# Performance work log

Measured on AMD Instinct MI355X. Metric: run time of the kernel, lower is better.

Reference implementation:

```python
import jax, jax.numpy as jnp
import numpy as np

B, S, H, NH = 4, 1024, 1024, 16
DH = H // NH
EPS = 1e-12  # BERT layer_norm_eps


def layer_norm(x, scale, bias, eps=EPS):
    mu = jnp.mean(x, axis=-1, keepdims=True)
    var = jnp.var(x, axis=-1, keepdims=True)
    return (x - mu) / jnp.sqrt(var + eps) * scale + bias


def setup_inputs() -> dict:
    key = jax.random.key(0)
    ks = jax.random.split(key, 8)
    lin = lambda k: jax.random.normal(k, (H, H), jnp.float32) * 0.02
    zeros_h = jnp.zeros((H,), jnp.float32)
    return {
        "hidden_states": jax.random.normal(ks[0], (B, S, H), jnp.float32),
        "group_prob": jnp.zeros((B, S, S), jnp.float32),
        "attention_mask": jnp.ones((B, 1, S, S), jnp.int32),
        "Wq": lin(ks[1]), "bq": zeros_h,
        "Wk": lin(ks[2]), "bk": zeros_h,
        "Wv": lin(ks[3]), "bv": zeros_h,
        "gWq": lin(ks[4]), "gbq": zeros_h,
        "gWk": lin(ks[5]), "gbk": zeros_h,
        "g_ln_scale": jnp.ones((H,), jnp.float32), "g_ln_bias": zeros_h,
        "Wo": lin(ks[6]), "bo": zeros_h,
        "out_ln_scale": jnp.ones((H,), jnp.float32), "out_ln_bias": zeros_h,
    }


def _forward(hidden_states, group_prob, attention_mask, Wq, bq, Wk, bk, Wv, bv,
             gWq, gbq, gWk, gbk, g_ln_scale, g_ln_bias, Wo, bo,
             out_ln_scale, out_ln_bias):
    am = attention_mask.astype(jnp.int32)              # [B,1,S,S]
    a = jnp.eye(S, k=1, dtype=jnp.int32)               # superdiagonal
    b = jnp.eye(S, dtype=jnp.int32)                    # identity
    c = jnp.eye(S, k=-1, dtype=jnp.int32)              # subdiagonal
    tri = jnp.triu(jnp.ones((S, S), jnp.float32))      # upper tri incl diag

    # ---- GroupAttention (tree-transformer constituent priors) ----
    hs = layer_norm(hidden_states, g_ln_scale, g_ln_bias)
    gq = hs @ gWq.T + gbq
    gk = hs @ gWk.T + gbk
    g_scores = jnp.einsum('bqd,bkd->bqk', gq, gk) / jnp.float32(H)
    g_mask = (am & (a + c))[:, 0]                      # [B,S,S] tridiag band, no diag
    g_scores = jnp.where(g_mask == 0, -jnp.inf, g_scores)
    n_attn = jnp.nan_to_num(jax.nn.softmax(g_scores, axis=-1))
    n_attn = jnp.sqrt(n_attn * jnp.swapaxes(n_attn, -1, -2) + 1e-9)
    n_attn = group_prob + (1.0 - group_prob) * n_attn  # prior mixing
    t = jnp.where(a == 0, 0.0, jnp.log(n_attn + 1e-9)) @ tri
    g_attn = jnp.exp(tri @ t)
    strict_upper = tri.astype(jnp.int32) - b           # nonzero on strict upper tri
    g_attn = jnp.where(strict_upper == 0, 0.0, g_attn)
    g_attn = g_attn + jnp.swapaxes(g_attn, -1, -2) + jnp.where(b == 0, 1e-9, n_attn)
    break_prob = n_attn

    # ---- BertSelfAttention, mode 'L' ----
    def split_heads(x):
        return x.reshape(B, S, NH, DH).transpose(0, 2, 1, 3)  # [B,NH,S,DH]
    q = split_heads(hidden_states @ Wq.T + bq)
    k = split_heads(hidden_states @ Wk.T + bk)
    v = split_heads(hidden_states @ Wv.T + bv)
    scores = jnp.einsum('bhqd,bhkd->bhqk', q, k) / jnp.sqrt(jnp.float32(DH))
    keep = (am | b) != 0                               # diag always attended
    scores = jnp.where(keep, scores, -jnp.inf)
    probs = jax.nn.softmax(scores, axis=-1)
    probs = probs * g_attn[:, None]                    # group-prob reweighting
    ctx = jnp.einsum('bhqk,bhkd->bhqd', probs, v)
    ctx = ctx.transpose(0, 2, 1, 3).reshape(B, S, H)

    # ---- BertSelfOutput: dense + residual + LayerNorm ----
    out = layer_norm(ctx @ Wo.T + bo + hidden_states, out_ln_scale, out_ln_bias)
    return out, scores, g_attn, break_prob


def reference(hidden_states, group_prob, attention_mask, Wq, bq, Wk, bk, Wv, bv,
              gWq, gbq, gWk, gbk, g_ln_scale, g_ln_bias, Wo, bo,
              out_ln_scale, out_ln_bias):
    return _forward(hidden_states, group_prob, attention_mask, Wq, bq, Wk, bk,
                    Wv, bv, gWq, gbq, gWk, gbk, g_ln_scale, g_ln_bias, Wo, bo,
                    out_ln_scale, out_ln_bias)
```

## Files before the change

kernel.cpp:

```cpp
#include <hip/hip_runtime.h>
#include <math.h>

#define BB 4
#define S 1024
#define H 1024
#define NHD 16
#define DH 64
#define LN_EPS 1e-12f
#define SQ9 3.1622776601683795e-5f
#define NEG_INF (-__builtin_inff())

typedef unsigned short u16;
typedef unsigned int u32;
using bfrag = __attribute__((ext_vector_type(8))) short;
using f32x4 = __attribute__((ext_vector_type(4))) float;

typedef __attribute__((address_space(1))) void void_g;
typedef __attribute__((address_space(3))) void void_l;

__device__ __forceinline__ void gload16(const void* g, void* l) {
  __builtin_amdgcn_global_load_lds((void_g*)g, (void_l*)l, 16, 0, 0);
}

__device__ __forceinline__ u16 f2bf(float f) {
  u32 u = __builtin_bit_cast(u32, f);
  u32 r = (u + 0x7fffu + ((u >> 16) & 1u)) >> 16;
  return (u16)r;
}
__device__ __forceinline__ float bf2f(u32 b) {
  u32 u = b << 16;
  return __builtin_bit_cast(float, u);
}

__device__ __forceinline__ float block_sum256(float v, float* buf) {
#pragma unroll
  for (int o = 32; o > 0; o >>= 1) v += __shfl_down(v, o);
  if ((threadIdx.x & 63) == 0) buf[threadIdx.x >> 6] = v;
  __syncthreads();
  float r = buf[0] + buf[1] + buf[2] + buf[3];
  __syncthreads();
  return r;
}

__global__ __launch_bounds__(256) void prep_kernel(
    const float* __restrict__ Wq, const float* __restrict__ Wk, const float* __restrict__ Wv,
    const float* __restrict__ gWq, const float* __restrict__ gWk,
    const float* __restrict__ hidden, const int* __restrict__ am,
    const float* __restrict__ glns, const float* __restrict__ glnb,
    u16* __restrict__ dstW, u32* __restrict__ amb, u16* __restrict__ hsbf) {
  __shared__ float buf[4];
  int bid = blockIdx.x;
  if (bid < 9216) {
    const int WQ = 262144;
    int i = bid * 256 + threadIdx.x;
    const float* src; int off;
    if      (i < 1 * WQ) { src = Wq;  off = 0; }
    else if (i < 2 * WQ) { src = Wk;  off = 1 * WQ; }
    else if (i < 3 * WQ) { src = Wv;  off = 2 * WQ; }
    else if (i < 4 * WQ) { src = gWq; off = 3 * WQ; }
    else if (i < 5 * WQ) { src = gWk; off = 4 * WQ; }
    else                 { src = hidden; off = 5 * WQ; }
    float4 v = reinterpret_cast<const float4*>(src)[i - off];
    u32 lo = (u32)f2bf(v.x) | ((u32)f2bf(v.y) << 16);
    u32 hi = (u32)f2bf(v.z) | ((u32)f2bf(v.w) << 16);
    reinterpret_cast<uint2*>(dstW)[i] = make_uint2(lo, hi);
  } else if (bid < 25600) {
    size_t t = (size_t)(bid - 9216) * 256 + threadIdx.x;
    int v = am[t] != 0;
    unsigned long long m = __ballot(v);
    int lane = threadIdx.x & 63;
    if (lane == 0)       amb[t >> 5] = (u32)m;
    else if (lane == 32) amb[t >> 5] = (u32)(m >> 32);
  } else {
    size_t row = bid - 25600;
    const float4 xv = reinterpret_cast<const float4*>(hidden + row * H)[threadIdx.x];
    float s  = xv.x + xv.y + xv.z + xv.w;
    float s2 = xv.x * xv.x + xv.y * xv.y + xv.z * xv.z + xv.w * xv.w;
    s  = block_sum256(s, buf);
    s2 = block_sum256(s2, buf);
    float mu  = s * (1.0f / H);
    float var = s2 * (1.0f / H) - mu * mu;
    float inv = rsqrtf(var + LN_EPS);
    const float4 sv = reinterpret_cast<const float4*>(glns)[threadIdx.x];
    const float4 bv = reinterpret_cast<const float4*>(glnb)[threadIdx.x];
    float o0 = (xv.x - mu) * inv * sv.x + bv.x;
    float o1 = (xv.y - mu) * inv * sv.y + bv.y;
    float o2 = (xv.z - mu) * inv * sv.z + bv.z;
    float o3 = (xv.w - mu) * inv * sv.w + bv.w;
    u32 lo = (u32)f2bf(o0) | ((u32)f2bf(o1) << 16);
    u32 hi = (u32)f2bf(o2) | ((u32)f2bf(o3) << 16);
    reinterpret_cast<uint2*>(hsbf + row * H)[threadIdx.x] = make_uint2(lo, hi);
  }
}

__global__ __launch_bounds__(256) void cast_wo_kernel(const float* __restrict__ Wo,
                                                      u16* __restrict__ dst) {
  int i = blockIdx.x * 256 + threadIdx.x;
  float4 v = reinterpret_cast<const float4*>(Wo)[i];
  u32 lo = (u32)f2bf(v.x) | ((u32)f2bf(v.y) << 16);
  u32 hi = (u32)f2bf(v.z) | ((u32)f2bf(v.w) << 16);
  reinterpret_cast<uint2*>(dst)[i] = make_uint2(lo, hi);
}

__global__ __launch_bounds__(256) void mega_gemm(
    const u16* __restrict__ hbf, const u16* __restrict__ hsbf,
    const u16* __restrict__ Wcat,
    const float* __restrict__ bq, const float* __restrict__ bk, const float* __restrict__ bv,
    const float* __restrict__ gbq, const float* __restrict__ gbk,
    u16* __restrict__ q, u16* __restrict__ k, u16* __restrict__ vt,
    u16* __restrict__ gq, u16* __restrict__ gk) {
  __shared__ __align__(16) u16 SM[32768];
  const int Kdim = H;
  int fid = blockIdx.x + blockIdx.y * 40;
  int swz = (fid & 7) * 160 + (fid >> 3);
  int lx = swz % 40, ly = swz / 40;
  int which = lx >> 3;
  const u16* A = (which < 3) ? hbf : hsbf;
  int rowBlk = ly * 128, colBlk = lx * 128;
  int tid = threadIdx.x, wid = tid >> 6, l = tid & 63;
  int dr = l >> 3, sl = l & 7;
  int co = (sl ^ dr) << 3;
  const u16* Ag = A + (size_t)rowBlk * Kdim;
  const u16* Bg = Wcat + (size_t)colBlk * Kdim;
  f32x4 acc[4][4];
#pragma unroll
  for (int i = 0; i < 4; ++i)
#pragma unroll
    for (int j = 0; j < 4; ++j) acc[i][j] = (f32x4){0.f, 0.f, 0.f, 0.f};
#pragma unroll
  for (int i = 0; i < 4; ++i) {
    int L = wid * 4 + i;
    gload16(Ag + (size_t)(L * 8 + dr) * Kdim + co, &SM[L * 512]);
    gload16(Bg + (size_t)(L * 8 + dr) * Kdim + co, &SM[16384 + L * 512]);
  }
  __syncthreads();
  int wm = wid >> 1, wn = wid & 1;
  const int nt = Kdim >> 6;
  int buf = 0;
  int sw = (l & 7) << 4;
  for (int t = 0; t < nt; ++t) {
    if (t + 1 < nt) {
      int k0 = (t + 1) << 6;
      int dstoff = (buf ^ 1) * 8192;
#pragma unroll
      for (int i = 0; i < 4; ++i) {
        int L = wid * 4 + i;
        gload16(Ag + (size_t)(L * 8 + dr) * Kdim + k0 + co, &SM[dstoff + L * 512]);
        gload16(Bg + (size_t)(L * 8 + dr) * Kdim + k0 + co, &SM[16384 + dstoff + L * 512]);
      }
    }
    const char* Ab = (const char*)&SM[buf * 8192];
    const char* Bb = (const char*)&SM[16384 + buf * 8192];
#pragma unroll
    for (int ks = 0; ks < 2; ++ks) {
      int kb = (ks * 64 + ((l >> 4) << 4)) ^ sw;
      bfrag af[4], bfv[4];
#pragma unroll
      for (int mi = 0; mi < 4; ++mi)
        af[mi] = *(const bfrag*)(Ab + (wm * 64 + mi * 16 + (l & 15)) * 128 + kb);
#pragma unroll
      for (int ni = 0; ni < 4; ++ni)
        bfv[ni] = *(const bfrag*)(Bb + (wn * 64 + ni * 16 + (l & 15)) * 128 + kb);
#pragma unroll
      for (int mi = 0; mi < 4; ++mi)
#pragma unroll
        for (int ni = 0; ni < 4; ++ni)
          acc[mi][ni] = __builtin_amdgcn_mfma_f32_16x16x32_bf16(af[mi], bfv[ni], acc[mi][ni], 0, 0, 0);
    }
    __syncthreads();
    buf ^= 1;
  }
  const float* bias = (which == 0) ? bq : (which == 1) ? bk : (which == 2) ? bv
                      : (which == 3) ? gbq : gbk;
  if (which == 2) {
    u16* T = SM;
#pragma unroll
    for (int mi = 0; mi < 4; ++mi) {
#pragma unroll
      for (int ni = 0; ni < 4; ++ni) {
        int c = wn * 64 + ni * 16 + (l & 15);
        float bvv = bias[(colBlk & 1023) + c];
        int tokb = wm * 64 + mi * 16 + ((l >> 4) << 2);
        u32 w0 = (u32)f2bf(acc[mi][ni][0] + bvv) | ((u32)f2bf(acc[mi][ni][1] + bvv) << 16);
        u32 w1 = (u32)f2bf(acc[mi][ni][2] + bvv) | ((u32)f2bf(acc[mi][ni][3] + bvv) << 16);
        *(u32*)&T[c * 144 + tokb]     = w0;
        *(u32*)&T[c * 144 + tokb + 2] = w1;
      }
    }
    __syncthreads();
    int col = tid >> 1, th = tid & 1;
    int g = (colBlk & 1023) + col;
    int bb = rowBlk >> 10;
    int s0 = (rowBlk & 1023) + th * 64;
    const uint4* src = (const uint4*)&T[col * 144 + th * 64];
    u16* dst = vt + ((size_t)(bb * 1024 + g)) * S + s0;
#pragma unroll
    for (int i = 0; i < 8; ++i) reinterpret_cast<uint4*>(dst)[i] = src[i];
  } else {
    u16* O = (which == 0) ? q : (which == 1) ? k : (which == 3) ? gq : gk;
#pragma unroll
    for (int mi = 0; mi < 4; ++mi) {
#pragma unroll
      for (int ni = 0; ni < 4; ++ni) {
        int col = (colBlk + wn * 64 + ni * 16 + (l & 15)) & 1023;
        float bvv = bias[col];
#pragma unroll
        for (int j = 0; j < 4; ++j) {
          int row = rowBlk + wm * 64 + mi * 16 + ((l >> 4) << 2) + j;
          O[(size_t)row * H + col] = f2bf(acc[mi][ni][j] + bvv);
        }
      }
    }
  }
}

__global__ __launch_bounds__(256) void gemm_dense(
    const u16* __restrict__ A, const u16* __restrict__ Bw,
    const float* __restrict__ bias, const float* __restrict__ resid,
    u16* __restrict__ C) {
  __shared__ __align__(16) u16 SM[32768];
  const int Kdim = H;
  int fid = blockIdx.x + blockIdx.y * 8;
  int swz = (fid & 7) * 32 + (fid >> 3);
  int lx = swz & 7, ly = swz >> 3;
  int rowBlk = ly * 128, colBlk = lx * 128;
  int tid = threadIdx.x, wid = tid >> 6, l = tid & 63;
  int dr = l >> 3, sl = l & 7;
  int co = (sl ^ dr) << 3;
  const u16* Ag = A + (size_t)rowBlk * Kdim;
  const u16* Bg = Bw + (size_t)colBlk * Kdim;
  f32x4 acc[4][4];
#pragma unroll
  for (int i = 0; i < 4; ++i)
#pragma unroll
    for (int j = 0; j < 4; ++j) acc[i][j] = (f32x4){0.f, 0.f, 0.f, 0.f};
#pragma unroll
  for (int i = 0; i < 4; ++i) {
    int L = wid * 4 + i;
    gload16(Ag + (size_t)(L * 8 + dr) * Kdim + co, &SM[L * 512]);
    gload16(Bg + (size_t)(L * 8 + dr) * Kdim + co, &SM[16384 + L * 512]);
  }
  __syncthreads();
  int wm = wid >> 1, wn = wid & 1;
  const int nt = Kdim >> 6;
  int buf = 0;
  int sw = (l & 7) << 4;
  for (int t = 0; t < nt; ++t) {
    if (t + 1 < nt) {
      int k0 = (t + 1) << 6;
      int dstoff = (buf ^ 1) * 8192;
#pragma unroll
      for (int i = 0; i < 4; ++i) {
        int L = wid * 4 + i;
        gload16(Ag + (size_t)(L * 8 + dr) * Kdim + k0 + co, &SM[dstoff + L * 512]);
        gload16(Bg + (size_t)(L * 8 + dr) * Kdim + k0 + co, &SM[16384 + dstoff + L * 512]);
      }
    }
    const char* Ab = (const char*)&SM[buf * 8192];
    const char* Bb = (const char*)&SM[16384 + buf * 8192];
#pragma unroll
    for (int ks = 0; ks < 2; ++ks) {
      int kb = (ks * 64 + ((l >> 4) << 4)) ^ sw;
      bfrag af[4], bfv[4];
#pragma unroll
      for (int mi = 0; mi < 4; ++mi)
        af[mi] = *(const bfrag*)(Ab + (wm * 64 + mi * 16 + (l & 15)) * 128 + kb);
#pragma unroll
      for (int ni = 0; ni < 4; ++ni)
        bfv[ni] = *(const bfrag*)(Bb + (wn * 64 + ni * 16 + (l & 15)) * 128 + kb);
#pragma unroll
      for (int mi = 0; mi < 4; ++mi)
#pragma unroll
        for (int ni = 0; ni < 4; ++ni)
          acc[mi][ni] = __builtin_amdgcn_mfma_f32_16x16x32_bf16(af[mi], bfv[ni], acc[mi][ni], 0, 0, 0);
    }
    __syncthreads();
    buf ^= 1;
  }
#pragma unroll
  for (int mi = 0; mi < 4; ++mi) {
#pragma unroll
    for (int ni = 0; ni < 4; ++ni) {
      int col = colBlk + wn * 64 + ni * 16 + (l & 15);
      float bvv = bias[col];
#pragma unroll
      for (int j = 0; j < 4; ++j) {
        int row = rowBlk + wm * 64 + mi * 16 + ((l >> 4) << 2) + j;
        C[(size_t)row * H + col] = f2bf(acc[mi][ni][j] + bvv + resid[(size_t)row * H + col]);
      }
    }
  }
}

__global__ __launch_bounds__(256) void band_dots_kernel(
    const u16* __restrict__ gq, const u16* __restrict__ gk,
    float* __restrict__ znext, float* __restrict__ zprev) {
  __shared__ float buf[4];
  size_t idx = blockIdx.x;
  int i = (int)(idx & (S - 1));
  uint2 q2 = reinterpret_cast<const uint2*>(gq + idx * H)[threadIdx.x];
  float q0 = bf2f(q2.x & 0xffff), q1 = bf2f(q2.x >> 16);
  float q2f = bf2f(q2.y & 0xffff), q3 = bf2f(q2.y >> 16);
  float dn = 0.f, dp = 0.f;
  if (i < S - 1) {
    uint2 k2 = reinterpret_cast<const uint2*>(gk + (idx + 1) * H)[threadIdx.x];
    dn = q0 * bf2f(k2.x & 0xffff) + q1 * bf2f(k2.x >> 16) +
         q2f * bf2f(k2.y & 0xffff) + q3 * bf2f(k2.y >> 16);
  }
  if (i > 0) {
    uint2 k2 = reinterpret_cast<const uint2*>(gk + (idx - 1) * H)[threadIdx.x];
    dp = q0 * bf2f(k2.x & 0xffff) + q1 * bf2f(k2.x >> 16) +
         q2f * bf2f(k2.y & 0xffff) + q3 * bf2f(k2.y >> 16);
  }
  dn = block_sum256(dn, buf);
  dp = block_sum256(dp, buf);
  if (threadIdx.x == 0) { znext[idx] = dn; zprev[idx] = dp; }
}

__global__ __launch_bounds__(1024) void band_prefix_kernel(
    const float* __restrict__ znext, const float* __restrict__ zprev,
    const int* __restrict__ am, const float* __restrict__ gp,
    float* __restrict__ sband, float* __restrict__ Cpre) {
  __shared__ float pd[S];
  __shared__ float scn[S];
  int b = blockIdx.x, i = threadIdx.x;
  size_t idx = (size_t)b * S + i;
  bool luv = (i < S - 1) && (am[((size_t)b * S + i) * S + i + 1] != 0);
  bool ldv = (i > 0) && (am[((size_t)b * S + i) * S + i - 1] != 0);
  float pf, pdn;
  if (!luv && !ldv) { pf = 0.f; pdn = 0.f; }
  else if (!ldv)    { pf = 1.f; pdn = 0.f; }
  else if (!luv)    { pf = 0.f; pdn = 1.f; }
  else {
    float lu = znext[idx] * (1.0f / (float)H);
    float ld = zprev[idx] * (1.0f / (float)H);
    float m = fmaxf(lu, ld);
    float eu = expf(lu - m), ed = expf(ld - m);
    float inv = 1.f / (eu + ed);
    pf = eu * inv; pdn = ed * inv;
  }
  pd[i] = pdn;
  __syncthreads();
  float sb = 0.f, L = 0.f;
  if (i < S - 1) {
    sb = sqrtf(pf * pd[i + 1] + 1e-9f);
    float gpv = gp[((size_t)b * S + i) * S + (i + 1)];
    float nm = gpv + (1.f - gpv) * sb;
    L = logf(nm + 1e-9f);
  }
  sband[idx] = sb;
  scn[i] = L;
  __syncthreads();
  for (int off = 1; off < S; off <<= 1) {
    float t = (i >= off) ? scn[i - off] : 0.f;
    __syncthreads();
    scn[i] += t;
    __syncthreads();
  }
  Cpre[idx] = (i > 0) ? scn[i - 1] : 0.f;
}

__global__ __launch_bounds__(256) void gattn_write_kernel(
    const float* __restrict__ gp, const float* __restrict__ sband,
    const float* __restrict__ Cpre, float* __restrict__ ga, float* __restrict__ brk) {
  __shared__ float Crow[S];
  __shared__ float Srow[S];
  size_t bi = blockIdx.x;
  int b = (int)(bi >> 10), i = (int)(bi & (S - 1));
  reinterpret_cast<float4*>(Crow)[threadIdx.x] =
      reinterpret_cast<const float4*>(Cpre + (size_t)b * S)[threadIdx.x];
  reinterpret_cast<float4*>(Srow)[threadIdx.x] =
      reinterpret_cast<const float4*>(sband + (size_t)b * S)[threadIdx.x];
  __syncthreads();
  float Ci = Crow[i];
  size_t rowoff = bi * S;
  const float4 g4 = reinterpret_cast<const float4*>(gp + rowoff)[threadIdx.x];
  const float gparr[4] = {g4.x, g4.y, g4.z, g4.w};
  float go[4], bo_[4];
#pragma unroll
  for (int j = 0; j < 4; ++j) {
    int k = threadIdx.x * 4 + j;
    float gpv = gparr[j];
    float gav;
    if (k == i) {
      gav = gpv + (1.f - gpv) * SQ9;
    } else {
      float d = (k > i) ? (Crow[k] - Ci) : (Ci - Crow[k]);
      gav = expf(d) + 1e-9f;
    }
    float sval = (k == i + 1) ? Srow[i] : ((k == i - 1) ? Srow[k] : SQ9);
    go[j]  = gav;
    bo_[j] = gpv + (1.f - gpv) * sval;
  }
  f32x4 go4 = (f32x4){go[0], go[1], go[2], go[3]};
  __builtin_nontemporal_store(go4, reinterpret_cast<f32x4*>(ga + rowoff) + threadIdx.x);
  f32x4 bo4 = (f32x4){bo_[0], bo_[1], bo_[2], bo_[3]};
  __builtin_nontemporal_store(bo4, reinterpret_cast<f32x4*>(brk + rowoff) + threadIdx.x);
}

__global__ __launch_bounds__(256) void flash_kernel(
    const u16* __restrict__ q, const u16* __restrict__ k, const u16* __restrict__ vt,
    const u32* __restrict__ amb, const float* __restrict__ Cpre,
    const float* __restrict__ gp,
    float* __restrict__ scores, u16* __restrict__ ctx) {
  __shared__ __align__(16) u16 Qt[4096];
  __shared__ __align__(16) u16 Kt[2][4096];
  __shared__ __align__(16) u16 Vt[2][4096];
  __shared__ __align__(16) u16 Pt[4096];
  __shared__ float CLds[1024];
  int fid = blockIdx.x + blockIdx.y * 16;
  int swz = (fid & 7) * 128 + (fid >> 3);
  int qb = swz & 15, bh = swz >> 4;
  int b = bh >> 4, h = bh & 15;
  int tid = threadIdx.x, wid = tid >> 6, l = tid & 63;
  int dr = l >> 3, sl = l & 7;
  int co = (sl ^ dr) << 3;
  const u16* qbase = q + ((size_t)b * S + qb * 64) * H + h * 64;
  const u16* kbase = k + (size_t)b * S * H + h * 64;
  const u16* vtb   = vt + (size_t)bh * 64 * S;
  reinterpret_cast<float4*>(CLds)[tid] =
      reinterpret_cast<const float4*>(Cpre + (size_t)b * S)[tid];
#pragma unroll
  for (int i = 0; i < 2; ++i) {
    int L = wid * 2 + i;
    gload16(qbase + (size_t)(L * 8 + dr) * H + co, &Qt[L * 512]);
    gload16(kbase + (size_t)(L * 8 + dr) * H + co, &Kt[0][L * 512]);
    gload16(vtb + (size_t)(L * 8 + dr) * S + co, &Vt[0][L * 512]);
  }
  __syncthreads();
  int sw = (l & 7) << 4;
  int qr = l & 15;
  bfrag qa[2];
#pragma unroll
  for (int ks = 0; ks < 2; ++ks) {
    int kb = (ks * 64 + ((l >> 4) << 4)) ^ sw;
    qa[ks] = *(const bfrag*)((const char*)Qt + (wid * 16 + qr) * 128 + kb);
  }
  int rowg0 = qb * 64 + wid * 16 + ((l >> 4) << 2);
  float Ci[4], gdiag[4];
#pragma unroll
  for (int j = 0; j < 4; ++j) {
    int row = rowg0 + j;
    Ci[j] = CLds[row];
    float gpd = gp[((size_t)b * S + row) * S + row];
    gdiag[j] = gpd + (1.f - gpd) * SQ9;
  }
  float m_run[4], l_run[4];
  f32x4 oacc[4];
#pragma unroll
  for (int j = 0; j < 4; ++j) { m_run[j] = NEG_INF; l_run[j] = 0.f; }
#pragma unroll
  for (int nb = 0; nb < 4; ++nb) oacc[nb] = (f32x4){0.f, 0.f, 0.f, 0.f};
  int buf = 0;
  for (int kt = 0; kt < 16; ++kt) {
    if (kt < 15) {
      const u16* kb2 = kbase + (size_t)((kt + 1) * 64) * H;
#pragma unroll
      for (int i = 0; i < 2; ++i) {
        int L = wid * 2 + i;
        gload16(kb2 + (size_t)(L * 8 + dr) * H + co, &Kt[buf ^ 1][L * 512]);
        gload16(vtb + (size_t)(L * 8 + dr) * S + (kt + 1) * 64 + co, &Vt[buf ^ 1][L * 512]);
      }
    }
    f32x4 acc[4];
#pragma unroll
    for (int nb = 0; nb < 4; ++nb) acc[nb] = (f32x4){0.f, 0.f, 0.f, 0.f};
#pragma unroll
    for (int ks = 0; ks < 2; ++ks) {
      int kb = (ks * 64 + ((l >> 4) << 4)) ^ sw;
#pragma unroll
      for (int nb = 0; nb < 4; ++nb) {
        bfrag bv = *(const bfrag*)((const char*)Kt[buf] + (nb * 16 + qr) * 128 + kb);
        acc[nb] = __builtin_amdgcn_mfma_f32_16x16x32_bf16(qa[ks], bv, acc[nb], 0, 0, 0);
      }
    }
    float vals[4][4];
    float tm[4] = {NEG_INF, NEG_INF, NEG_INF, NEG_INF};
#pragma unroll
    for (int j = 0; j < 4; ++j) {
      int row = rowg0 + j;
      const u32* amw = amb + ((size_t)b * S + row) * 32 + kt * 2;
      u32 w0 = amw[0], w1 = amw[1];
      float* srow = scores + ((size_t)bh * S + row) * S + kt * 64;
#pragma unroll
      for (int nb = 0; nb < 4; ++nb) {
        int col = nb * 16 + qr;
        int colg = kt * 64 + col;
        u32 word = (nb < 2) ? w0 : w1;
        int keep = (int)((word >> (col & 31)) & 1u) | (row == colg);
        float v = keep ? acc[nb][j] * 0.125f : NEG_INF;
        vals[nb][j] = v;
        __builtin_nontemporal_store(v, srow + col);
        tm[j] = fmaxf(tm[j], v);
      }
    }
#pragma unroll
    for (int j = 0; j < 4; ++j) {
#pragma unroll
      for (int o = 1; o < 16; o <<= 1) tm[j] = fmaxf(tm[j], __shfl_xor(tm[j], o));
    }
    float Ck[4];
#pragma unroll
    for (int nb = 0; nb < 4; ++nb) Ck[nb] = CLds[kt * 64 + nb * 16 + qr];
#pragma unroll
    for (int j = 0; j < 4; ++j) {
      int row = rowg0 + j;
      int prow = wid * 16 + ((l >> 4) << 2) + j;
      char* ptrow = (char*)Pt + prow * 128;
      int psw = (prow & 7) << 4;
      float mn = fmaxf(m_run[j], tm[j]);
      float p[4];
      float sc = 1.f, lsum = 0.f;
      if (mn > NEG_INF) {
        sc = expf(m_run[j] - mn);
#pragma unroll
        for (int nb = 0; nb < 4; ++nb) p[nb] = expf(vals[nb][j] - mn);
        lsum = p[0] + p[1] + p[2] + p[3];
      } else {
#pragma unroll
        for (int nb = 0; nb < 4; ++nb) p[nb] = 0.f;
      }
#pragma unroll
      for (int o = 1; o < 16; o <<= 1) lsum += __shfl_xor(lsum, o);
      m_run[j] = mn;
      l_run[j] = l_run[j] * sc + lsum;
#pragma unroll
      for (int nb = 0; nb < 4; ++nb) {
        int colg = kt * 64 + nb * 16 + qr;
        bool isdiag = (colg == row);
        float d = (colg > row) ? (Ck[nb] - Ci[j]) : (Ci[j] - Ck[nb]);
        float gaval = isdiag ? gdiag[j] : expf(d);
        float pg = p[nb] * gaval;
        *(u16*)(ptrow + (((nb * 16 + qr) * 2) ^ psw)) = f2bf(pg);
        oacc[nb][j] *= sc;
      }
    }
#pragma unroll
    for (int ks = 0; ks < 2; ++ks) {
      int kb = (ks * 64 + ((l >> 4) << 4)) ^ sw;
      bfrag pa = *(const bfrag*)((const char*)Pt + (wid * 16 + qr) * 128 + kb);
#pragma unroll
      for (int nb = 0; nb < 4; ++nb) {
        bfrag vv = *(const bfrag*)((const char*)Vt[buf] + (nb * 16 + qr) * 128 + kb);
        oacc[nb] = __builtin_amdgcn_mfma_f32_16x16x32_bf16(pa, vv, oacc[nb], 0, 0, 0);
      }
    }
    __syncthreads();
    buf ^= 1;
  }
#pragma unroll
  for (int j = 0; j < 4; ++j) {
    int row = rowg0 + j;
    float ir = 1.f / l_run[j];
#pragma unroll
    for (int nb = 0; nb < 4; ++nb) {
      int d = nb * 16 + qr;
      ctx[((size_t)b * S + row) * H + h * 64 + d] = f2bf(oacc[nb][j] * ir);
    }
  }
}

__global__ __launch_bounds__(256) void ln_bf_kernel(
    const u16* __restrict__ x, const float* __restrict__ sc,
    const float* __restrict__ bi, float* __restrict__ y) {
  __shared__ float buf[4];
  size_t row = blockIdx.x;
  uint2 xv = reinterpret_cast<const uint2*>(x + row * H)[threadIdx.x];
  float x0 = bf2f(xv.x & 0xffff), x1 = bf2f(xv.x >> 16);
  float x2 = bf2f(xv.y & 0xffff), x3 = bf2f(xv.y >> 16);
  float s  = x0 + x1 + x2 + x3;
  float s2 = x0 * x0 + x1 * x1 + x2 * x2 + x3 * x3;
  s  = block_sum256(s, buf);
  s2 = block_sum256(s2, buf);
  float mu  = s * (1.0f / H);
  float var = s2 * (1.0f / H) - mu * mu;
  float inv = rsqrtf(var + LN_EPS);
  const float4 sv = reinterpret_cast<const float4*>(sc)[threadIdx.x];
  const float4 bv = reinterpret_cast<const float4*>(bi)[threadIdx.x];
  float4 o;
  o.x = (x0 - mu) * inv * sv.x + bv.x;
  o.y = (x1 - mu) * inv * sv.y + bv.y;
  o.z = (x2 - mu) * inv * sv.z + bv.z;
  o.w = (x3 - mu) * inv * sv.w + bv.w;
  reinterpret_cast<float4*>(y + row * H)[threadIdx.x] = o;
}

extern "C" void kernel_launch(void* const* d_in, const int* in_sizes, int n_in,
                              void* d_out, int out_size, void* d_ws, size_t ws_size,
                              hipStream_t stream) {
  const float* hidden = (const float*)d_in[0];
  const float* gp     = (const float*)d_in[1];
  const int*   am     = (const int*)d_in[2];
  const float* Wq = (const float*)d_in[3];  const float* bq = (const float*)d_in[4];
  const float* Wk = (const float*)d_in[5];  const float* bk = (const float*)d_in[6];
  const float* Wv = (const float*)d_in[7];  const float* bv = (const float*)d_in[8];
  const float* gWq = (const float*)d_in[9]; const float* gbq = (const float*)d_in[10];
  const float* gWk = (const float*)d_in[11];const float* gbk = (const float*)d_in[12];
  const float* glns = (const float*)d_in[13]; const float* glnb = (const float*)d_in[14];
  const float* Wo = (const float*)d_in[15]; const float* bo = (const float*)d_in[16];
  const float* olns = (const float*)d_in[17]; const float* olnb = (const float*)d_in[18];

  float* out    = (float*)d_out;
  float* scores = out + (size_t)BB * S * H;
  float* gattn  = scores + (size_t)BB * NHD * S * S;
  float* brk    = gattn + (size_t)BB * S * S;

  const size_t MB = 1u << 20;
  char* w = (char*)d_ws;
  u16* Wcat  = (u16*)(w);
  u16* hbf   = (u16*)(w + 10 * MB);
  u16* ctxbf = hbf;
  u16* hsbf  = (u16*)(w + 18 * MB);
  u16* Wobf  = hsbf;
  u16* qbf   = (u16*)(w + 26 * MB);
  u16* kbf   = (u16*)(w + 34 * MB);
  u16* vtb   = (u16*)(w + 42 * MB);
  u16* gqbf  = (u16*)(w + 50 * MB);
  u16* densebf = gqbf;
  u16* gkbf  = (u16*)(w + 58 * MB);
  u32* amb   = (u32*)(w + 66 * MB);
  float* znext  = (float*)(w + 66 * MB + 512 * 1024);
  float* zprev  = znext + BB * S;
  float* sbandA = zprev + BB * S;
  float* CpreA  = sbandA + BB * S;

  dim3 blk(256);

  prep_kernel<<<29696, blk, 0, stream>>>(Wq, Wk, Wv, gWq, gWk, hidden, am,
                                         glns, glnb, Wcat, amb, hsbf);

  mega_gemm<<<dim3(40, 32), blk, 0, stream>>>(hbf, hsbf, Wcat,
                                              bq, bk, bv, gbq, gbk,
                                              qbf, kbf, vtb, gqbf, gkbf);
  cast_wo_kernel<<<1024, blk, 0, stream>>>(Wo, Wobf);

  band_dots_kernel<<<BB * S, blk, 0, stream>>>(gqbf, gkbf, znext, zprev);
  band_prefix_kernel<<<BB, 1024, 0, stream>>>(znext, zprev, am, gp, sbandA, CpreA);
  gattn_write_kernel<<<BB * S, blk, 0, stream>>>(gp, sbandA, CpreA, gattn, brk);

  flash_kernel<<<dim3(16, 64), blk, 0, stream>>>(qbf, kbf, vtb, amb, CpreA, gp,
                                                 scores, ctxbf);

  gemm_dense<<<dim3(8, 32), blk, 0, stream>>>(ctxbf, Wobf, bo, hidden, densebf);
  ln_bf_kernel<<<BB * S, blk, 0, stream>>>(densebf, olns, olnb, out);
}
```

Before: 273.5 us.

## Fuse group-attention and break-prob writes into flash kernel head-0 blocks

Removes the separate gattn_write kernel. The flash-attention blocks for head 0 of each batch now compute and write g_attn and break_prob rows tile by tile alongside their attention work. The block-to-tile mapping changes so that the head-0 blocks, which carry the extra work, are scheduled first. This saves one kernel launch and overlaps the memory-bound output writes with compute-bound attention. The cost is load imbalance: 64 blocks do extra global traffic and exp work, and shared memory per block grows.

```diff
diff --git a/kernel.cpp b/kernel.cpp
--- a/kernel.cpp
+++ b/kernel.cpp
@@ -360,57 +360,28 @@
   Cpre[idx] = (i > 0) ? scn[i - 1] : 0.f;
 }
 
-__global__ __launch_bounds__(256) void gattn_write_kernel(
-    const float* __restrict__ gp, const float* __restrict__ sband,
-    const float* __restrict__ Cpre, float* __restrict__ ga, float* __restrict__ brk) {
-  __shared__ float Crow[S];
-  __shared__ float Srow[S];
-  size_t bi = blockIdx.x;
-  int b = (int)(bi >> 10), i = (int)(bi & (S - 1));
-  reinterpret_cast<float4*>(Crow)[threadIdx.x] =
-      reinterpret_cast<const float4*>(Cpre + (size_t)b * S)[threadIdx.x];
-  reinterpret_cast<float4*>(Srow)[threadIdx.x] =
-      reinterpret_cast<const float4*>(sband + (size_t)b * S)[threadIdx.x];
-  __syncthreads();
-  float Ci = Crow[i];
-  size_t rowoff = bi * S;
-  const float4 g4 = reinterpret_cast<const float4*>(gp + rowoff)[threadIdx.x];
-  const float gparr[4] = {g4.x, g4.y, g4.z, g4.w};
-  float go[4], bo_[4];
-#pragma unroll
-  for (int j = 0; j < 4; ++j) {
-    int k = threadIdx.x * 4 + j;
-    float gpv = gparr[j];
-    float gav;
-    if (k == i) {
-      gav = gpv + (1.f - gpv) * SQ9;
-    } else {
-      float d = (k > i) ? (Crow[k] - Ci) : (Ci - Crow[k]);
-      gav = expf(d) + 1e-9f;
-    }
-    float sval = (k == i + 1) ? Srow[i] : ((k == i - 1) ? Srow[k] : SQ9);
-    go[j]  = gav;
-    bo_[j] = gpv + (1.f - gpv) * sval;
-  }
-  f32x4 go4 = (f32x4){go[0], go[1], go[2], go[3]};
-  __builtin_nontemporal_store(go4, reinterpret_cast<f32x4*>(ga + rowoff) + threadIdx.x);
-  f32x4 bo4 = (f32x4){bo_[0], bo_[1], bo_[2], bo_[3]};
-  __builtin_nontemporal_store(bo4, reinterpret_cast<f32x4*>(brk + rowoff) + threadIdx.x);
-}
-
 __global__ __launch_bounds__(256) void flash_kernel(
     const u16* __restrict__ q, const u16* __restrict__ k, const u16* __restrict__ vt,
     const u32* __restrict__ amb, const float* __restrict__ Cpre,
-    const float* __restrict__ gp,
-    float* __restrict__ scores, u16* __restrict__ ctx) {
+    const float* __restrict__ sband, const float* __restrict__ gp,
+    float* __restrict__ scores, u16* __restrict__ ctx,
+    float* __restrict__ ga, float* __restrict__ brk) {
   __shared__ __align__(16) u16 Qt[4096];
   __shared__ __align__(16) u16 Kt[2][4096];
   __shared__ __align__(16) u16 Vt[2][4096];
   __shared__ __align__(16) u16 Pt[4096];
   __shared__ float CLds[1024];
+  __shared__ float SLds[1024];
   int fid = blockIdx.x + blockIdx.y * 16;
-  int swz = (fid & 7) * 128 + (fid >> 3);
-  int qb = swz & 15, bh = swz >> 4;
+  int qb, bh;
+  if (fid < 64) {
+    bh = (fid >> 4) << 4;  qb = fid & 15;
+  } else {
+    int r = fid - 64;
+    int hh = 1 + (r >> 6);
+    bh = (((r >> 4) & 3) << 4) + hh;
+    qb = r & 15;
+  }
   int b = bh >> 4, h = bh & 15;
   int tid = threadIdx.x, wid = tid >> 6, l = tid & 63;
   int dr = l >> 3, sl = l & 7;
@@ -420,6 +391,9 @@
   const u16* vtb   = vt + (size_t)bh * 64 * S;
   reinterpret_cast<float4*>(CLds)[tid] =
       reinterpret_cast<const float4*>(Cpre + (size_t)b * S)[tid];
+  if (h == 0)
+    reinterpret_cast<float4*>(SLds)[tid] =
+        reinterpret_cast<const float4*>(sband + (size_t)b * S)[tid];
 #pragma unroll
   for (int i = 0; i < 2; ++i) {
     int L = wid * 2 + i;
@@ -445,6 +419,12 @@
     float gpd = gp[((size_t)b * S + row) * S + row];
     gdiag[j] = gpd + (1.f - gpd) * SQ9;
   }
+  int erow = qb * 64 + (tid >> 2);
+  float eCi = CLds[erow];
+  float eScur = SLds[erow];
+  float eSprev = SLds[(erow > 0) ? erow - 1 : 0];
+  float egpd = 0.f;
+  if (h == 0) egpd = gp[((size_t)b * S + erow) * S + erow];
   float m_run[4], l_run[4];
   f32x4 oacc[4];
 #pragma unroll
@@ -533,6 +513,36 @@
         float pg = p[nb] * gaval;
         *(u16*)(ptrow + (((nb * 16 + qr) * 2) ^ psw)) = f2bf(pg);
         oacc[nb][j] *= sc;
+      }
+    }
+    if (h == 0) {
+      const float* gprow = gp + ((size_t)b * S + erow) * S + kt * 64;
+      float* garow = ga + ((size_t)b * S + erow) * S + kt * 64;
+      float* brow  = brk + ((size_t)b * S + erow) * S + kt * 64;
+#pragma unroll
+      for (int c4 = 0; c4 < 4; ++c4) {
+        int kb0 = c4 * 16 + (tid & 3) * 4;
+        float4 gp4 = *reinterpret_cast<const float4*>(gprow + kb0);
+        const float gpa[4] = {gp4.x, gp4.y, gp4.z, gp4.w};
+        float go[4], bo[4];
+#pragma unroll
+        for (int j = 0; j < 4; ++j) {
+          int kg = kt * 64 + kb0 + j;
+          float gav;
+          if (kg == erow) {
+            gav = egpd + (1.f - egpd) * SQ9;
+          } else {
+            float dd = (kg > erow) ? (CLds[kg] - eCi) : (eCi - CLds[kg]);
+            gav = expf(dd) + 1e-9f;
+          }
+          float sval = (kg == erow + 1) ? eScur : ((kg == erow - 1) ? eSprev : SQ9);
+          go[j] = gav;
+          bo[j] = gpa[j] + (1.f - gpa[j]) * sval;
+        }
+        f32x4 go4 = (f32x4){go[0], go[1], go[2], go[3]};
+        f32x4 bo4 = (f32x4){bo[0], bo[1], bo[2], bo[3]};
+        __builtin_nontemporal_store(go4, reinterpret_cast<f32x4*>(garow + kb0));
+        __builtin_nontemporal_store(bo4, reinterpret_cast<f32x4*>(brow + kb0));
       }
     }
 #pragma unroll
@@ -636,10 +646,10 @@
 
   band_dots_kernel<<<BB * S, blk, 0, stream>>>(gqbf, gkbf, znext, zprev);
   band_prefix_kernel<<<BB, 1024, 0, stream>>>(znext, zprev, am, gp, sbandA, CpreA);
-  gattn_write_kernel<<<BB * S, blk, 0, stream>>>(gp, sbandA, CpreA, gattn, brk);
-
-  flash_kernel<<<dim3(16, 64), blk, 0, stream>>>(qbf, kbf, vtb, amb, CpreA, gp,
-                                                 scores, ctxbf);
+
+  flash_kernel<<<dim3(16, 64), blk, 0, stream>>>(qbf, kbf, vtb, amb, CpreA,
+                                                 sbandA, gp, scores, ctxbf,
+                                                 gattn, brk);
 
   gemm_dense<<<dim3(8, 32), blk, 0, stream>>>(ctxbf, Wobf, bo, hidden, densebf);
   ln_bf_kernel<<<BB * S, blk, 0, stream>>>(densebf, olns, olnb, out);
```

New measurement: 285.4 us. +4.3%, slower.

## Cut flash kernel LDS footprint, use exp2 math, defer row-sum reduction

Applied to the files above, without the earlier changes.

Shrinks shared memory in the flash attention kernel by aliasing the Q and P tiles and single-buffering V, which is now loaded each iteration and waited on before the PV matmul. Launch bounds request 4 blocks per CU to raise occupancy. Softmax and the group-attention exponentials are fused into one exp2 per element, with C prescaled by log2(e), and the per-iteration cross-lane sum of row totals is deferred to after the loop. It also adds setprio around the MFMA sections and a vectorized mask-word load. The cost is that V loads are no longer prefetched a tile ahead, so their latency is exposed, and an extra barrier is added each iteration.

```diff
diff --git a/kernel.cpp b/kernel.cpp
--- a/kernel.cpp
+++ b/kernel.cpp
@@ -9,6 +9,7 @@
 #define LN_EPS 1e-12f
 #define SQ9 3.1622776601683795e-5f
 #define NEG_INF (-__builtin_inff())
+#define L2E 1.4426950408889634f
 
 typedef unsigned short u16;
 typedef unsigned int u32;
@@ -398,15 +399,14 @@
   __builtin_nontemporal_store(bo4, reinterpret_cast<f32x4*>(brk + rowoff) + threadIdx.x);
 }
 
-__global__ __launch_bounds__(256) void flash_kernel(
+__global__ __launch_bounds__(256, 4) void flash_kernel(
     const u16* __restrict__ q, const u16* __restrict__ k, const u16* __restrict__ vt,
     const u32* __restrict__ amb, const float* __restrict__ Cpre,
     const float* __restrict__ gp,
     float* __restrict__ scores, u16* __restrict__ ctx) {
-  __shared__ __align__(16) u16 Qt[4096];
+  __shared__ __align__(16) u16 QPt[4096];
   __shared__ __align__(16) u16 Kt[2][4096];
-  __shared__ __align__(16) u16 Vt[2][4096];
-  __shared__ __align__(16) u16 Pt[4096];
+  __shared__ __align__(16) u16 Vt[4096];
   __shared__ float CLds[1024];
   int fid = blockIdx.x + blockIdx.y * 16;
   int swz = (fid & 7) * 128 + (fid >> 3);
@@ -418,14 +418,16 @@
   const u16* qbase = q + ((size_t)b * S + qb * 64) * H + h * 64;
   const u16* kbase = k + (size_t)b * S * H + h * 64;
   const u16* vtb   = vt + (size_t)bh * 64 * S;
-  reinterpret_cast<float4*>(CLds)[tid] =
-      reinterpret_cast<const float4*>(Cpre + (size_t)b * S)[tid];
+  {
+    float4 c4 = reinterpret_cast<const float4*>(Cpre + (size_t)b * S)[tid];
+    c4.x *= L2E; c4.y *= L2E; c4.z *= L2E; c4.w *= L2E;
+    reinterpret_cast<float4*>(CLds)[tid] = c4;
+  }
 #pragma unroll
   for (int i = 0; i < 2; ++i) {
     int L = wid * 2 + i;
-    gload16(qbase + (size_t)(L * 8 + dr) * H + co, &Qt[L * 512]);
+    gload16(qbase + (size_t)(L * 8 + dr) * H + co, &QPt[L * 512]);
     gload16(kbase + (size_t)(L * 8 + dr) * H + co, &Kt[0][L * 512]);
-    gload16(vtb + (size_t)(L * 8 + dr) * S + co, &Vt[0][L * 512]);
   }
   __syncthreads();
   int sw = (l & 7) << 4;
@@ -434,59 +436,65 @@
 #pragma unroll
   for (int ks = 0; ks < 2; ++ks) {
     int kb = (ks * 64 + ((l >> 4) << 4)) ^ sw;
-    qa[ks] = *(const bfrag*)((const char*)Qt + (wid * 16 + qr) * 128 + kb);
-  }
+    qa[ks] = *(const bfrag*)((const char*)QPt + (wid * 16 + qr) * 128 + kb);
+  }
+  __syncthreads();
   int rowg0 = qb * 64 + wid * 16 + ((l >> 4) << 2);
-  float Ci[4], gdiag[4];
+  float Ci2[4], gdiag[4];
 #pragma unroll
   for (int j = 0; j < 4; ++j) {
     int row = rowg0 + j;
-    Ci[j] = CLds[row];
+    Ci2[j] = CLds[row];
     float gpd = gp[((size_t)b * S + row) * S + row];
     gdiag[j] = gpd + (1.f - gpd) * SQ9;
   }
-  float m_run[4], l_run[4];
+  float m_run[4], l_loc[4];
   f32x4 oacc[4];
 #pragma unroll
-  for (int j = 0; j < 4; ++j) { m_run[j] = NEG_INF; l_run[j] = 0.f; }
+  for (int j = 0; j < 4; ++j) { m_run[j] = NEG_INF; l_loc[j] = 0.f; }
 #pragma unroll
   for (int nb = 0; nb < 4; ++nb) oacc[nb] = (f32x4){0.f, 0.f, 0.f, 0.f};
-  int buf = 0;
+  int cur = 0;
   for (int kt = 0; kt < 16; ++kt) {
+#pragma unroll
+    for (int i = 0; i < 2; ++i) {
+      int L = wid * 2 + i;
+      gload16(vtb + (size_t)(L * 8 + dr) * S + kt * 64 + co, &Vt[L * 512]);
+    }
     if (kt < 15) {
       const u16* kb2 = kbase + (size_t)((kt + 1) * 64) * H;
 #pragma unroll
       for (int i = 0; i < 2; ++i) {
         int L = wid * 2 + i;
-        gload16(kb2 + (size_t)(L * 8 + dr) * H + co, &Kt[buf ^ 1][L * 512]);
-        gload16(vtb + (size_t)(L * 8 + dr) * S + (kt + 1) * 64 + co, &Vt[buf ^ 1][L * 512]);
+        gload16(kb2 + (size_t)(L * 8 + dr) * H + co, &Kt[cur ^ 1][L * 512]);
       }
     }
     f32x4 acc[4];
 #pragma unroll
     for (int nb = 0; nb < 4; ++nb) acc[nb] = (f32x4){0.f, 0.f, 0.f, 0.f};
+    __builtin_amdgcn_s_setprio(1);
 #pragma unroll
     for (int ks = 0; ks < 2; ++ks) {
       int kb = (ks * 64 + ((l >> 4) << 4)) ^ sw;
 #pragma unroll
       for (int nb = 0; nb < 4; ++nb) {
-        bfrag bv = *(const bfrag*)((const char*)Kt[buf] + (nb * 16 + qr) * 128 + kb);
+        bfrag bv = *(const bfrag*)((const char*)Kt[cur] + (nb * 16 + qr) * 128 + kb);
         acc[nb] = __builtin_amdgcn_mfma_f32_16x16x32_bf16(qa[ks], bv, acc[nb], 0, 0, 0);
       }
     }
+    __builtin_amdgcn_s_setprio(0);
     float vals[4][4];
     float tm[4] = {NEG_INF, NEG_INF, NEG_INF, NEG_INF};
 #pragma unroll
     for (int j = 0; j < 4; ++j) {
       int row = rowg0 + j;
-      const u32* amw = amb + ((size_t)b * S + row) * 32 + kt * 2;
-      u32 w0 = amw[0], w1 = amw[1];
+      uint2 w01 = *reinterpret_cast<const uint2*>(amb + ((size_t)b * S + row) * 32 + kt * 2);
       float* srow = scores + ((size_t)bh * S + row) * S + kt * 64;
 #pragma unroll
       for (int nb = 0; nb < 4; ++nb) {
         int col = nb * 16 + qr;
         int colg = kt * 64 + col;
-        u32 word = (nb < 2) ? w0 : w1;
+        u32 word = (nb < 2) ? w01.x : w01.y;
         int keep = (int)((word >> (col & 31)) & 1u) | (row == colg);
         float v = keep ? acc[nb][j] * 0.125f : NEG_INF;
         vals[nb][j] = v;
@@ -499,59 +507,70 @@
 #pragma unroll
       for (int o = 1; o < 16; o <<= 1) tm[j] = fmaxf(tm[j], __shfl_xor(tm[j], o));
     }
-    float Ck[4];
-#pragma unroll
-    for (int nb = 0; nb < 4; ++nb) Ck[nb] = CLds[kt * 64 + nb * 16 + qr];
+    float Ck2[4];
+#pragma unroll
+    for (int nb = 0; nb < 4; ++nb) Ck2[nb] = CLds[kt * 64 + nb * 16 + qr];
 #pragma unroll
     for (int j = 0; j < 4; ++j) {
       int row = rowg0 + j;
       int prow = wid * 16 + ((l >> 4) << 2) + j;
-      char* ptrow = (char*)Pt + prow * 128;
+      char* ptrow = (char*)QPt + prow * 128;
       int psw = (prow & 7) << 4;
       float mn = fmaxf(m_run[j], tm[j]);
-      float p[4];
-      float sc = 1.f, lsum = 0.f;
+      float pp[4], pg[4];
+      float sc;
       if (mn > NEG_INF) {
-        sc = expf(m_run[j] - mn);
-#pragma unroll
-        for (int nb = 0; nb < 4; ++nb) p[nb] = expf(vals[nb][j] - mn);
-        lsum = p[0] + p[1] + p[2] + p[3];
+        sc = exp2f((m_run[j] - mn) * L2E);
+        float m2 = mn * L2E;
+#pragma unroll
+        for (int nb = 0; nb < 4; ++nb) {
+          float t = __builtin_fmaf(vals[nb][j], L2E, -m2);
+          pp[nb] = exp2f(t);
+          int colg = kt * 64 + nb * 16 + qr;
+          float d2 = (colg > row) ? (Ck2[nb] - Ci2[j]) : (Ci2[j] - Ck2[nb]);
+          float g = exp2f(t + d2);
+          pg[nb] = (colg == row) ? pp[nb] * gdiag[j] : g;
+        }
       } else {
-#pragma unroll
-        for (int nb = 0; nb < 4; ++nb) p[nb] = 0.f;
-      }
-#pragma unroll
-      for (int o = 1; o < 16; o <<= 1) lsum += __shfl_xor(lsum, o);
+        sc = 1.f;
+#pragma unroll
+        for (int nb = 0; nb < 4; ++nb) { pp[nb] = 0.f; pg[nb] = 0.f; }
+      }
       m_run[j] = mn;
-      l_run[j] = l_run[j] * sc + lsum;
+      l_loc[j] = l_loc[j] * sc + (pp[0] + pp[1] + pp[2] + pp[3]);
 #pragma unroll
       for (int nb = 0; nb < 4; ++nb) {
-        int colg = kt * 64 + nb * 16 + qr;
-        bool isdiag = (colg == row);
-        float d = (colg > row) ? (Ck[nb] - Ci[j]) : (Ci[j] - Ck[nb]);
-        float gaval = isdiag ? gdiag[j] : expf(d);
-        float pg = p[nb] * gaval;
-        *(u16*)(ptrow + (((nb * 16 + qr) * 2) ^ psw)) = f2bf(pg);
+        *(u16*)(ptrow + (((nb * 16 + qr) * 2) ^ psw)) = f2bf(pg[nb]);
         oacc[nb][j] *= sc;
       }
     }
+    asm volatile("s_waitcnt vmcnt(0)" ::: "memory");
+    __builtin_amdgcn_sched_barrier(0);
+    __builtin_amdgcn_s_barrier();
+    __builtin_amdgcn_s_setprio(1);
 #pragma unroll
     for (int ks = 0; ks < 2; ++ks) {
       int kb = (ks * 64 + ((l >> 4) << 4)) ^ sw;
-      bfrag pa = *(const bfrag*)((const char*)Pt + (wid * 16 + qr) * 128 + kb);
+      bfrag pa = *(const bfrag*)((const char*)QPt + (wid * 16 + qr) * 128 + kb);
 #pragma unroll
       for (int nb = 0; nb < 4; ++nb) {
-        bfrag vv = *(const bfrag*)((const char*)Vt[buf] + (nb * 16 + qr) * 128 + kb);
+        bfrag vv = *(const bfrag*)((const char*)Vt + (nb * 16 + qr) * 128 + kb);
         oacc[nb] = __builtin_amdgcn_mfma_f32_16x16x32_bf16(pa, vv, oacc[nb], 0, 0, 0);
       }
     }
+    __builtin_amdgcn_s_setprio(0);
     __syncthreads();
-    buf ^= 1;
+    cur ^= 1;
+  }
+#pragma unroll
+  for (int j = 0; j < 4; ++j) {
+#pragma unroll
+    for (int o = 1; o < 16; o <<= 1) l_loc[j] += __shfl_xor(l_loc[j], o);
   }
 #pragma unroll
   for (int j = 0; j < 4; ++j) {
     int row = rowg0 + j;
-    float ir = 1.f / l_run[j];
+    float ir = 1.f / l_loc[j];
 #pragma unroll
     for (int nb = 0; nb < 4; ++nb) {
       int d = nb * 16 + qr;
```

Result: slower. 342.4 us (+25.2%).
